# Kernel tuning notes

Hardware: AMD Instinct MI355X
Metric: run time of the kernel (lower is better)

The kernel has to match this reference:

```python
import jax, jax.numpy as jnp
import numpy as np
from jax import lax

V, E, Q, D = 100000, 300, 64, 4096
K = 5
NEG_SLOPE = 0.01


def setup_inputs() -> dict:
    key = jax.random.key(0)
    ks = jax.random.split(key, 16)
    return {
        "question": jax.random.randint(ks[0], (Q,), 0, V),
        "doc1": jax.random.randint(ks[1], (D,), 0, V),
        "doc2": jax.random.randint(ks[2], (D,), 0, V),
        "doc1_sim": jax.random.uniform(ks[3], (D, Q), dtype=jnp.float32),
        "doc2_sim": jax.random.uniform(ks[4], (D, Q), dtype=jnp.float32),
        "gaf": jax.random.normal(ks[5], (4,), dtype=jnp.float32),
        "baf": jax.random.normal(ks[6], (4,), dtype=jnp.float32),
        "emb": jax.random.normal(ks[7], (V, E), dtype=jnp.float32) * 0.1,
        "idf": jax.random.uniform(ks[8], (V, 1), dtype=jnp.float32) * 10.0,
        "conv_w": jax.random.normal(ks[9], (E, E, 3), dtype=jnp.float32) * (1.0 / np.sqrt(3 * E)),
        "conv_b": jax.random.normal(ks[10], (E,), dtype=jnp.float32) * 0.01,
        "qw_w": jax.random.normal(ks[11], (1, E + 1), dtype=jnp.float32) * (1.0 / np.sqrt(E + 1)),
        "qw_b": jax.random.normal(ks[12], (1,), dtype=jnp.float32) * 0.01,
        "lin1_w": jax.random.normal(ks[13], (8, 6), dtype=jnp.float32) * (1.0 / np.sqrt(6)),
        "lin2_w": jax.random.normal(ks[14], (1, 8), dtype=jnp.float32) * (1.0 / np.sqrt(8)),
        "out_w": jax.random.normal(ks[15], (1, 5), dtype=jnp.float32) * (1.0 / np.sqrt(5)),
    }


def _leaky(x):
    return jnp.where(x >= 0, x, NEG_SLOPE * x)


def _conv_residual(x, w, b):
    # x: [L, E]. Torch Conv1d(E,E,3,padding=2) followed by slice [1:L+1] is a
    # centered SAME conv; activation applied before the residual add.
    y = lax.conv_general_dilated(x.T[None], w, (1,), [(1, 1)],
                                 dimension_numbers=("NCW", "OIW", "NCW"))
    y = y[0] + b[:, None]            # [E, L]
    return _leaky(y).T + x           # [L, E]


def _cosine(A, B):
    # A: [Q, E], B: [L, E] -> [Q, L]
    num = A @ B.T
    den = jnp.linalg.norm(A, axis=-1)[:, None] * jnp.linalg.norm(B, axis=-1)[None, :]
    return num / den


def _kmax_pool(sim):
    # sim: [Q, L] -> [Q, 2] = (max, mean of top-K)
    top = lax.top_k(sim, K)[0]       # descending [Q, K]
    return jnp.stack([top[:, 0], jnp.mean(top, axis=-1)], axis=-1)


def _get_output(pooled_list, q_weights, lin1_w, lin2_w):
    temp = jnp.concatenate(pooled_list, axis=-1)     # [Q, 6]
    lo = _leaky(temp @ lin1_w.T) @ lin2_w.T          # [Q, 1]
    lo = lo[:, 0] * q_weights
    return jnp.sum(lo) / lo.shape[0]


def reference(question, doc1, doc2, doc1_sim, doc2_sim, gaf, baf,
              emb, idf, conv_w, conv_b, qw_w, qw_b, lin1_w, lin2_w, out_w):
    q_emb = emb[question]            # [Q, E]
    d1_emb = emb[doc1]               # [D, E]
    d2_emb = emb[doc2]

    sim_ins_d1 = _cosine(q_emb, d1_emb)
    sim_ins_d2 = _cosine(q_emb, d2_emb)

    q_conv = _conv_residual(q_emb, conv_w, conv_b)
    d1_conv = _conv_residual(d1_emb, conv_w, conv_b)
    d2_conv = _conv_residual(d2_emb, conv_w, conv_b)

    sim_sen_d1 = _cosine(q_conv, d1_conv)
    sim_sen_d2 = _cosine(q_conv, d2_conv)

    sim_oh_d1 = doc1_sim.T           # [Q, D]
    sim_oh_d2 = doc2_sim.T

    p_oh_d1, p_ins_d1, p_sen_d1 = _kmax_pool(sim_oh_d1), _kmax_pool(sim_ins_d1), _kmax_pool(sim_sen_d1)
    p_oh_d2, p_ins_d2, p_sen_d2 = _kmax_pool(sim_oh_d2), _kmax_pool(sim_ins_d2), _kmax_pool(sim_sen_d2)

    q_idfs = idf[question]           # [Q, 1]
    qw = jnp.concatenate([q_conv, q_idfs], axis=-1) @ qw_w.T + qw_b  # [Q, 1]
    q_weights = jax.nn.softmax(qw[:, 0], axis=-1)

    doc1_emit = _get_output([p_oh_d1, p_ins_d1, p_sen_d1], q_weights, lin1_w, lin2_w)
    doc2_emit = _get_output([p_oh_d2, p_ins_d2, p_sen_d2], q_weights, lin1_w, lin2_w)

    good_feats = jnp.concatenate([gaf, doc1_emit[None]])  # [5]
    bad_feats = jnp.concatenate([baf, doc2_emit[None]])
    good_out = out_w @ good_feats                          # [1]
    bad_out = out_w @ bad_feats

    loss1 = jnp.mean(jnp.maximum(0.0, -(good_out - bad_out) + 1.0))
    return (loss1, good_out, bad_out, loss1, loss1)
```

## Files before the change

kernel.cpp:

```cpp
#include <hip/hip_runtime.h>
#include <math.h>

#define EE 300
#define KP 320
#define LDSW 328
#define QQ 64
#define DD 4096
#define NEG 0.01f

typedef __attribute__((ext_vector_type(8))) short short8;
typedef __attribute__((ext_vector_type(4))) float f32x4;
typedef unsigned short ushort_t;

__device__ inline ushort_t f2bf(float f) {
  unsigned u = __builtin_bit_cast(unsigned, f);
  u += 0x7fff + ((u >> 16) & 1);
  return (ushort_t)(u >> 16);
}
__device__ inline float bf2f(ushort_t h) {
  return __builtin_bit_cast(float, (unsigned)h << 16);
}
__device__ inline void top5_insert(float* t, float v) {
  if (v > t[4]) {
    t[4] = v;
    #pragma unroll
    for (int j = 4; j > 0; --j)
      if (t[j] > t[j - 1]) { float tmp = t[j]; t[j] = t[j - 1]; t[j - 1] = tmp; }
  }
}

#define GATHER_ROWS (66 + 4098 + 4098)
#define GATHER_BLOCKS ((GATHER_ROWS + 3) / 4)
#define WT_BLOCKS 143
#define OHPOOL_BLOCKS 256
#define PREP_BLOCKS (GATHER_BLOCKS + WT_BLOCKS + OHPOOL_BLOCKS)

__global__ __launch_bounds__(256) void prep(
    const float* __restrict__ emb, const int* __restrict__ question,
    const int* __restrict__ doc1, const int* __restrict__ doc2,
    const float* __restrict__ conv_w,
    const float* __restrict__ doc1_sim, const float* __restrict__ doc2_sim,
    ushort_t* __restrict__ qbe, ushort_t* __restrict__ d1be, ushort_t* __restrict__ d2be,
    ushort_t* __restrict__ qbc, ushort_t* __restrict__ d1bc, ushort_t* __restrict__ d2bc,
    ushort_t* __restrict__ wt2,
    float* __restrict__ nq2, float* __restrict__ nd12, float* __restrict__ nd22,
    float* __restrict__ pt5) {
  __shared__ float strip[64][33];
  int b = blockIdx.x;
  int tid = threadIdx.x;
  int wv = tid >> 6, lane = tid & 63;
  if (b < GATHER_BLOCKS) {
    int g = b * 4 + wv;
    if (g >= GATHER_ROWS) return;
    int t, row;
    if (g < 66)             { t = 0; row = g; }
    else if (g < 66 + 4098) { t = 1; row = g - 66; }
    else                    { t = 2; row = g - 4164; }
    const int* idx = t == 0 ? question : (t == 1 ? doc1 : doc2);
    int L = t == 0 ? QQ : DD;
    ushort_t* be = t == 0 ? qbe : (t == 1 ? d1be : d2be);
    ushort_t* bc = t == 0 ? qbc : (t == 1 ? d1bc : d2bc);
    float* nrm2 = t == 0 ? nq2 : (t == 1 ? nd12 : nd22);
    const short8 z8 = (short8){0, 0, 0, 0, 0, 0, 0, 0};
    if (row == 0 || row == L + 1) {
      if (lane < 40) *(short8*)(be + (size_t)row * KP + lane * 8) = z8;
      return;
    }
    int r = row - 1;
    const float* src = emb + (size_t)idx[r] * EE;
    float ss = 0.f;
    if (lane < 37) {
      f32x4 v0 = *(const f32x4*)(src + lane * 8);
      f32x4 v1 = *(const f32x4*)(src + lane * 8 + 4);
      short8 hb;
      #pragma unroll
      for (int e = 0; e < 4; ++e) { hb[e] = (short)f2bf(v0[e]); ss += v0[e] * v0[e]; }
      #pragma unroll
      for (int e = 0; e < 4; ++e) { hb[4 + e] = (short)f2bf(v1[e]); ss += v1[e] * v1[e]; }
      *(short8*)(be + (size_t)row * KP + lane * 8) = hb;
    } else if (lane == 37) {
      f32x4 v0 = *(const f32x4*)(src + 296);
      short8 hb = z8;
      #pragma unroll
      for (int e = 0; e < 4; ++e) { hb[e] = (short)f2bf(v0[e]); ss += v0[e] * v0[e]; }
      *(short8*)(be + (size_t)row * KP + 296) = hb;
    } else if (lane < 40) {
      *(short8*)(be + (size_t)row * KP + lane * 8) = z8;
    }
    if (lane < 20) bc[(size_t)r * KP + 300 + lane] = 0;
    #pragma unroll
    for (int o = 32; o; o >>= 1) ss += __shfl_xor(ss, o);
    if (lane == 0) nrm2[r] = ss;
  } else if (b < GATHER_BLOCKS + WT_BLOCKS) {
    int f = (b - GATHER_BLOCKS) * 4 + wv;
    if (f >= 570) return;
    int ks = f % 10, n = (f / 10) % 19, tap = f / 190;
    int o = n * 16 + (lane & 15);
    int kbase = ks * 32 + (lane >> 4) * 8;
    ushort_t* dst = wt2 + (size_t)f * 512 + lane * 8;
    #pragma unroll
    for (int e = 0; e < 8; ++e) {
      int k = kbase + e;
      float v = (o < EE && k < EE) ? conv_w[((size_t)o * EE + k) * 3 + tap] : 0.f;
      dst[e] = f2bf(v);
    }
  } else {
    int ob = b - (GATHER_BLOCKS + WT_BLOCKS);
    int o = ob >> 7, chunk = ob & 127;
    int ps = o ? 3 : 0;
    const float* dsim = o ? doc2_sim : doc1_sim;
    int l0 = chunk * 32;
    int r = tid >> 3, q0 = (tid & 7) * 8;
    const float* srcp = dsim + (size_t)(l0 + r) * QQ + q0;
    f32x4 v0 = *(const f32x4*)srcp;
    f32x4 v1 = *(const f32x4*)(srcp + 4);
    #pragma unroll
    for (int e = 0; e < 4; ++e) strip[q0 + e][r] = v0[e];
    #pragma unroll
    for (int e = 0; e < 4; ++e) strip[q0 + 4 + e][r] = v1[e];
    __syncthreads();
    if (tid < 64) {
      float t5[5] = {-1e30f, -1e30f, -1e30f, -1e30f, -1e30f};
      #pragma unroll
      for (int l = 0; l < 32; ++l) top5_insert(t5, strip[tid][l]);
      float* dst = pt5 + (((size_t)ps * QQ + tid) * 128 + chunk) * 8;
      *(f32x4*)dst = (f32x4){t5[0], t5[1], t5[2], t5[3]};
      *(f32x4*)(dst + 4) = (f32x4){t5[4], -1e30f, -1e30f, -1e30f};
    }
  }
}

__global__ __launch_bounds__(256) void conv_mfma(
    const ushort_t* __restrict__ wt2, const float* __restrict__ bias,
    const float* __restrict__ qw_w,
    const ushort_t* __restrict__ qbe, const ushort_t* __restrict__ d1be,
    const ushort_t* __restrict__ d2be,
    ushort_t* __restrict__ qbc, ushort_t* __restrict__ d1bc,
    ushort_t* __restrict__ d2bc,
    float* __restrict__ nqcH, float* __restrict__ nd1cH, float* __restrict__ nd2cH,
    float* __restrict__ qwaccH) {
  __shared__ ushort_t lds[34 * LDSW];
  __shared__ float normbuf[4][32];
  __shared__ float qwbuf[4][32];
  int bx = blockIdx.x;
  int t, m0, yh;
  if (bx < 4) { t = 0; m0 = (bx >> 1) * 32; yh = bx & 1; }
  else {
    int i = bx - 4;
    t = 1 + (i >> 8);
    int j = i & 255;
    m0 = (j >> 1) * 32; yh = j & 1;
  }
  const ushort_t* be = t == 0 ? qbe : (t == 1 ? d1be : d2be);
  ushort_t* bc = t == 0 ? qbc : (t == 1 ? d1bc : d2bc);
  float* ncH = t == 0 ? nqcH : (t == 1 ? nd1cH : nd2cH);
  int ncs = t == 0 ? QQ : DD;
  int tid = threadIdx.x;
  for (int s = tid; s < 34 * 40; s += 256) {
    int row = s / 40, col = s - row * 40;
    *(short8*)(&lds[row * LDSW + col * 8]) =
        *(const short8*)(be + (size_t)(m0 + row) * KP + col * 8);
  }
  __syncthreads();
  int wv = tid >> 6, lane = tid & 63, mrow = lane & 15, g = lane >> 4;
  int nstart, ncnt;
  if (yh == 0) { nstart = (wv < 2) ? 3 * wv : 2 * wv + 2; ncnt = (wv < 2) ? 3 : 2; }
  else         { nstart = (wv == 0) ? 10 : 2 * wv + 11;   ncnt = (wv == 0) ? 3 : 2; }
  f32x4 acc[3][2];
  #pragma unroll
  for (int j = 0; j < 3; ++j)
    #pragma unroll
    for (int h = 0; h < 2; ++h) acc[j][h] = (f32x4){0.f, 0.f, 0.f, 0.f};

  for (int tap = 0; tap < 3; ++tap) {
    const ushort_t* alo = &lds[(mrow + tap) * LDSW + g * 8];
    #pragma unroll
    for (int ks = 0; ks < 10; ++ks) {
      short8 a0 = *(const short8*)(alo + ks * 32);
      short8 a1 = *(const short8*)(alo + 16 * LDSW + ks * 32);
      #pragma unroll
      for (int j = 0; j < 3; ++j) {
        if (j < ncnt) {
          short8 bfr = *(const short8*)(wt2 +
              (size_t)((tap * 19 + nstart + j) * 10 + ks) * 512 + lane * 8);
          acc[j][0] = __builtin_amdgcn_mfma_f32_16x16x32_bf16(a0, bfr, acc[j][0], 0, 0, 0);
          acc[j][1] = __builtin_amdgcn_mfma_f32_16x16x32_bf16(a1, bfr, acc[j][1], 0, 0, 0);
        }
      }
    }
  }
  float ss[2][4] = {{0.f,0.f,0.f,0.f},{0.f,0.f,0.f,0.f}};
  float yq[2][4] = {{0.f,0.f,0.f,0.f},{0.f,0.f,0.f,0.f}};
  #pragma unroll
  for (int j = 0; j < 3; ++j) {
    if (j < ncnt) {
      int col = (nstart + j) * 16 + mrow;
      if (col < EE) {
        float bcol = bias[col];
        float qwc = (t == 0) ? qw_w[col] : 0.f;
        #pragma unroll
        for (int h = 0; h < 2; ++h) {
          #pragma unroll
          for (int r = 0; r < 4; ++r) {
            int lrow = h * 16 + g * 4 + r;
            float y = acc[j][h][r] + bcol;
            y = (y >= 0.f) ? y : NEG * y;
            y += bf2f(lds[(1 + lrow) * LDSW + col]);
            bc[(size_t)(m0 + lrow) * KP + col] = f2bf(y);
            ss[h][r] += y * y;
            if (t == 0) yq[h][r] += y * qwc;
          }
        }
      }
    }
  }
  #pragma unroll
  for (int h = 0; h < 2; ++h) {
    #pragma unroll
    for (int r = 0; r < 4; ++r) {
      float s = ss[h][r];
      s += __shfl_xor(s, 1); s += __shfl_xor(s, 2);
      s += __shfl_xor(s, 4); s += __shfl_xor(s, 8);
      float sq = yq[h][r];
      sq += __shfl_xor(sq, 1); sq += __shfl_xor(sq, 2);
      sq += __shfl_xor(sq, 4); sq += __shfl_xor(sq, 8);
      if (mrow == 0) {
        normbuf[wv][h * 16 + g * 4 + r] = s;
        qwbuf[wv][h * 16 + g * 4 + r] = sq;
      }
    }
  }
  __syncthreads();
  if (tid < 32) {
    ncH[(size_t)yh * ncs + m0 + tid] =
        normbuf[0][tid] + normbuf[1][tid] + normbuf[2][tid] + normbuf[3][tid];
    if (t == 0)
      qwaccH[yh * QQ + m0 + tid] =
          qwbuf[0][tid] + qwbuf[1][tid] + qwbuf[2][tid] + qwbuf[3][tid];
  }
}

__global__ __launch_bounds__(256) void sim_pool(
    const ushort_t* __restrict__ qbe, const ushort_t* __restrict__ d1be,
    const ushort_t* __restrict__ d2be,
    const ushort_t* __restrict__ qbc, const ushort_t* __restrict__ d1bc,
    const ushort_t* __restrict__ d2bc,
    const float* __restrict__ nq2, const float* __restrict__ nd12,
    const float* __restrict__ nd22, const float* __restrict__ nqcH,
    const float* __restrict__ nd1cH, const float* __restrict__ nd2cH,
    float* __restrict__ pt5) {
  __shared__ ushort_t ldsB[32 * LDSW];
  __shared__ float strip[64][33];
  int s = blockIdx.x >> 7, chunk = blockIdx.x & 127;
  int ps = (s == 0) ? 1 : (s == 1) ? 4 : (s == 2) ? 2 : 5;
  int l0 = chunk * 32;
  const ushort_t* A = (s < 2) ? qbe + KP : qbc;
  const ushort_t* B = s == 0 ? d1be + KP : s == 1 ? d2be + KP
                    : s == 2 ? d1bc : d2bc;
  int tid = threadIdx.x;
  for (int i = tid; i < 32 * 40; i += 256) {
    int row = i / 40, col = i - row * 40;
    *(short8*)(&ldsB[row * LDSW + col * 8]) =
        *(const short8*)(B + (size_t)(l0 + row) * KP + col * 8);
  }
  __syncthreads();
  int wv = tid >> 6, lane = tid & 63, mrow = lane & 15, g = lane >> 4;
  f32x4 acc[2];
  acc[0] = (f32x4){0.f, 0.f, 0.f, 0.f};
  acc[1] = (f32x4){0.f, 0.f, 0.f, 0.f};
  const ushort_t* arow = A + (size_t)(wv * 16 + mrow) * KP + g * 8;
  #pragma unroll
  for (int ks = 0; ks < 10; ++ks) {
    short8 a = *(const short8*)(arow + ks * 32);
    #pragma unroll
    for (int n = 0; n < 2; ++n) {
      short8 bfr = *(const short8*)(&ldsB[(n * 16 + mrow) * LDSW + g * 8 + ks * 32]);
      acc[n] = __builtin_amdgcn_mfma_f32_16x16x32_bf16(a, bfr, acc[n], 0, 0, 0);
    }
  }
  #pragma unroll
  for (int n = 0; n < 2; ++n) {
    int l = n * 16 + mrow;
    float nb2v = (s == 0) ? nd12[l0 + l]
               : (s == 1) ? nd22[l0 + l]
               : (s == 2) ? (nd1cH[l0 + l] + nd1cH[DD + l0 + l])
                          : (nd2cH[l0 + l] + nd2cH[DD + l0 + l]);
    float inb = rsqrtf(nb2v);
    #pragma unroll
    for (int r = 0; r < 4; ++r) {
      int q = wv * 16 + g * 4 + r;
      float na2v = (s < 2) ? nq2[q] : (nqcH[q] + nqcH[QQ + q]);
      strip[q][l] = acc[n][r] * rsqrtf(na2v) * inb;
    }
  }
  __syncthreads();
  if (tid < 64) {
    float t5[5] = {-1e30f, -1e30f, -1e30f, -1e30f, -1e30f};
    #pragma unroll
    for (int l = 0; l < 32; ++l) top5_insert(t5, strip[tid][l]);
    float* dst = pt5 + (((size_t)ps * QQ + tid) * 128 + chunk) * 8;
    *(f32x4*)dst = (f32x4){t5[0], t5[1], t5[2], t5[3]};
    *(f32x4*)(dst + 4) = (f32x4){t5[4], -1e30f, -1e30f, -1e30f};
  }
}

__global__ __launch_bounds__(256) void merge(
    const float* __restrict__ pt5, float* __restrict__ pool) {
  int widx = blockIdx.x * 4 + (threadIdx.x >> 6);
  int lane = threadIdx.x & 63;
  int src = widx >> 6, q = widx & 63;
  const float* p0 = pt5 + (((size_t)src * QQ + q) * 128 + 2 * lane) * 8;
  float t5[5] = {-1e30f, -1e30f, -1e30f, -1e30f, -1e30f};
  #pragma unroll
  for (int c = 0; c < 2; ++c)
    #pragma unroll
    for (int j = 0; j < 5; ++j) top5_insert(t5, p0[c * 8 + j]);
  #pragma unroll
  for (int mask = 1; mask < 64; mask <<= 1) {
    float a[5], bb[5];
    #pragma unroll
    for (int j = 0; j < 5; ++j) { a[j] = t5[j]; bb[j] = __shfl_xor(t5[j], mask); }
    int ia = 0, ib = 0;
    #pragma unroll
    for (int j = 0; j < 5; ++j) t5[j] = (a[ia] >= bb[ib]) ? a[ia++] : bb[ib++];
  }
  if (lane == 0) {
    float sm = t5[0] + t5[1] + t5[2] + t5[3] + t5[4];
    pool[((size_t)src * QQ + q) * 2 + 0] = t5[0];
    pool[((size_t)src * QQ + q) * 2 + 1] = sm * 0.2f;
  }
}

__global__ void final_kernel(
    const float* __restrict__ qwaccH, const float* __restrict__ idf,
    const int* __restrict__ question, const float* __restrict__ qw_w,
    const float* __restrict__ qw_b, const float* __restrict__ pool,
    const float* __restrict__ lin1_w, const float* __restrict__ lin2_w,
    const float* __restrict__ out_w, const float* __restrict__ gaf,
    const float* __restrict__ baf, float* __restrict__ out5) {
  int q = threadIdx.x;
  float s = qwaccH[q] + qwaccH[QQ + q] + qw_b[0] + idf[question[q]] * qw_w[EE];
  float m = s;
  #pragma unroll
  for (int o = 32; o; o >>= 1) m = fmaxf(m, __shfl_xor(m, o));
  float e = expf(s - m);
  float se = e;
  #pragma unroll
  for (int o = 32; o; o >>= 1) se += __shfl_xor(se, o);
  float qwgt = e / se;

  float emit[2];
  for (int doc = 0; doc < 2; ++doc) {
    float temp[6];
    #pragma unroll
    for (int j = 0; j < 3; ++j) {
      temp[2 * j]     = pool[(((size_t)doc * 3 + j) * QQ + q) * 2 + 0];
      temp[2 * j + 1] = pool[(((size_t)doc * 3 + j) * QQ + q) * 2 + 1];
    }
    float lo = 0.f;
    #pragma unroll
    for (int r = 0; r < 8; ++r) {
      float h = 0.f;
      #pragma unroll
      for (int c = 0; c < 6; ++c) h += lin1_w[r * 6 + c] * temp[c];
      h = (h >= 0.f) ? h : NEG * h;
      lo += lin2_w[r] * h;
    }
    lo *= qwgt;
    #pragma unroll
    for (int o = 32; o; o >>= 1) lo += __shfl_xor(lo, o);
    emit[doc] = lo / (float)QQ;
  }
  if (q == 0) {
    float good = out_w[0] * gaf[0] + out_w[1] * gaf[1] + out_w[2] * gaf[2] +
                 out_w[3] * gaf[3] + out_w[4] * emit[0];
    float bad  = out_w[0] * baf[0] + out_w[1] * baf[1] + out_w[2] * baf[2] +
                 out_w[3] * baf[3] + out_w[4] * emit[1];
    float l1 = fmaxf(0.f, -(good - bad) + 1.f);
    out5[0] = l1; out5[1] = good; out5[2] = bad; out5[3] = l1; out5[4] = l1;
  }
}

extern "C" void kernel_launch(void* const* d_in, const int* in_sizes, int n_in,
                              void* d_out, int out_size, void* d_ws, size_t ws_size,
                              hipStream_t stream) {
  (void)in_sizes; (void)n_in; (void)out_size; (void)ws_size;
  const int* question   = (const int*)d_in[0];
  const int* doc1       = (const int*)d_in[1];
  const int* doc2       = (const int*)d_in[2];
  const float* doc1_sim = (const float*)d_in[3];
  const float* doc2_sim = (const float*)d_in[4];
  const float* gaf      = (const float*)d_in[5];
  const float* baf      = (const float*)d_in[6];
  const float* emb      = (const float*)d_in[7];
  const float* idf      = (const float*)d_in[8];
  const float* conv_w   = (const float*)d_in[9];
  const float* conv_b   = (const float*)d_in[10];
  const float* qw_w     = (const float*)d_in[11];
  const float* qw_b     = (const float*)d_in[12];
  const float* lin1_w   = (const float*)d_in[13];
  const float* lin2_w   = (const float*)d_in[14];
  const float* out_w    = (const float*)d_in[15];
  float* out = (float*)d_out;

  char* p = (char*)d_ws;
  ushort_t* qbe  = (ushort_t*)p; p += (size_t)(QQ + 2) * KP * 2;
  ushort_t* d1be = (ushort_t*)p; p += (size_t)(DD + 2) * KP * 2;
  ushort_t* d2be = (ushort_t*)p; p += (size_t)(DD + 2) * KP * 2;
  ushort_t* qbc  = (ushort_t*)p; p += (size_t)QQ * KP * 2;
  ushort_t* d1bc = (ushort_t*)p; p += (size_t)DD * KP * 2;
  ushort_t* d2bc = (ushort_t*)p; p += (size_t)DD * KP * 2;
  ushort_t* wt2  = (ushort_t*)p; p += (size_t)570 * 512 * 2;
  float* nq2    = (float*)p; p += QQ * 4;
  float* nd12   = (float*)p; p += DD * 4;
  float* nd22   = (float*)p; p += DD * 4;
  float* nqcH   = (float*)p; p += 2 * QQ * 4;
  float* nd1cH  = (float*)p; p += 2 * DD * 4;
  float* nd2cH  = (float*)p; p += 2 * DD * 4;
  float* qwaccH = (float*)p; p += 2 * QQ * 4;
  float* pt5    = (float*)p; p += (size_t)6 * QQ * 128 * 8 * 4;
  float* pool   = (float*)p; p += 6 * QQ * 2 * 4;

  prep<<<PREP_BLOCKS, 256, 0, stream>>>(
      emb, question, doc1, doc2, conv_w, doc1_sim, doc2_sim,
      qbe, d1be, d2be, qbc, d1bc, d2bc, wt2,
      nq2, nd12, nd22, pt5);

  conv_mfma<<<516, 256, 0, stream>>>(
      wt2, conv_b, qw_w, qbe, d1be, d2be, qbc, d1bc, d2bc,
      nqcH, nd1cH, nd2cH, qwaccH);

  sim_pool<<<512, 256, 0, stream>>>(
      qbe, d1be, d2be, qbc, d1bc, d2bc,
      nq2, nd12, nd22, nqcH, nd1cH, nd2cH, pt5);

  merge<<<96, 256, 0, stream>>>(pt5, pool);

  final_kernel<<<1, 64, 0, stream>>>(qwaccH, idf, question, qw_w, qw_b, pool,
                                     lin1_w, lin2_w, out_w, gaf, baf, out);
}
```

Before: 59.01 us.

## Retile conv MFMA blocks to 64 rows by quarter of output columns

The conv kernel now gives each block 64 sequence rows and one quarter of the output channels (5 N-tiles) instead of 32 rows and half the channels. Each wave reuses every weight fragment across four row tiles, which cuts global weight reads per MFMA, at the cost of one wave carrying a fifth tile alone and so an imbalanced load. Partial norm and qw sums are now split into four pieces that downstream kernels add together. LDS use grows to hold 66 rows.

Measured after the change: 61.77 us. +4.7%, slower.

```diff
diff --git a/kernel.cpp b/kernel.cpp
--- a/kernel.cpp
+++ b/kernel.cpp
@@ -137,69 +137,74 @@
     const ushort_t* __restrict__ d2be,
     ushort_t* __restrict__ qbc, ushort_t* __restrict__ d1bc,
     ushort_t* __restrict__ d2bc,
-    float* __restrict__ nqcH, float* __restrict__ nd1cH, float* __restrict__ nd2cH,
-    float* __restrict__ qwaccH) {
-  __shared__ ushort_t lds[34 * LDSW];
-  __shared__ float normbuf[4][32];
-  __shared__ float qwbuf[4][32];
+    float* __restrict__ nqcQ, float* __restrict__ nd1cQ, float* __restrict__ nd2cQ,
+    float* __restrict__ qwaccQ) {
+  __shared__ ushort_t lds[66 * LDSW];
+  __shared__ float normbuf[4][64];
+  __shared__ float qwbuf[4][64];
   int bx = blockIdx.x;
-  int t, m0, yh;
-  if (bx < 4) { t = 0; m0 = (bx >> 1) * 32; yh = bx & 1; }
+  int t, m0, yq;
+  if (bx < 4) { t = 0; m0 = 0; yq = bx; }
   else {
     int i = bx - 4;
     t = 1 + (i >> 8);
     int j = i & 255;
-    m0 = (j >> 1) * 32; yh = j & 1;
+    m0 = (j >> 2) * 64; yq = j & 3;
   }
   const ushort_t* be = t == 0 ? qbe : (t == 1 ? d1be : d2be);
   ushort_t* bc = t == 0 ? qbc : (t == 1 ? d1bc : d2bc);
-  float* ncH = t == 0 ? nqcH : (t == 1 ? nd1cH : nd2cH);
-  int ncs = t == 0 ? QQ : DD;
+  float* ncQ = t == 0 ? nqcQ : (t == 1 ? nd1cQ : nd2cQ);
+  int L = t == 0 ? QQ : DD;
   int tid = threadIdx.x;
-  for (int s = tid; s < 34 * 40; s += 256) {
+  for (int s = tid; s < 66 * 40; s += 256) {
     int row = s / 40, col = s - row * 40;
     *(short8*)(&lds[row * LDSW + col * 8]) =
         *(const short8*)(be + (size_t)(m0 + row) * KP + col * 8);
   }
   __syncthreads();
   int wv = tid >> 6, lane = tid & 63, mrow = lane & 15, g = lane >> 4;
-  int nstart, ncnt;
-  if (yh == 0) { nstart = (wv < 2) ? 3 * wv : 2 * wv + 2; ncnt = (wv < 2) ? 3 : 2; }
-  else         { nstart = (wv == 0) ? 10 : 2 * wv + 11;   ncnt = (wv == 0) ? 3 : 2; }
-  f32x4 acc[3][2];
-  #pragma unroll
-  for (int j = 0; j < 3; ++j)
-    #pragma unroll
-    for (int h = 0; h < 2; ++h) acc[j][h] = (f32x4){0.f, 0.f, 0.f, 0.f};
+  int nt0 = yq * 5 + wv;
+  int nt1 = yq * 5 + 4;
+  bool v1 = (wv == 0) && (nt1 <= 18);
+  f32x4 acc[2][4];
+  #pragma unroll
+  for (int j = 0; j < 2; ++j)
+    #pragma unroll
+    for (int h = 0; h < 4; ++h) acc[j][h] = (f32x4){0.f, 0.f, 0.f, 0.f};
 
   for (int tap = 0; tap < 3; ++tap) {
     const ushort_t* alo = &lds[(mrow + tap) * LDSW + g * 8];
     #pragma unroll
     for (int ks = 0; ks < 10; ++ks) {
-      short8 a0 = *(const short8*)(alo + ks * 32);
-      short8 a1 = *(const short8*)(alo + 16 * LDSW + ks * 32);
-      #pragma unroll
-      for (int j = 0; j < 3; ++j) {
-        if (j < ncnt) {
-          short8 bfr = *(const short8*)(wt2 +
-              (size_t)((tap * 19 + nstart + j) * 10 + ks) * 512 + lane * 8);
-          acc[j][0] = __builtin_amdgcn_mfma_f32_16x16x32_bf16(a0, bfr, acc[j][0], 0, 0, 0);
-          acc[j][1] = __builtin_amdgcn_mfma_f32_16x16x32_bf16(a1, bfr, acc[j][1], 0, 0, 0);
-        }
+      short8 a[4];
+      #pragma unroll
+      for (int h = 0; h < 4; ++h)
+        a[h] = *(const short8*)(alo + h * 16 * LDSW + ks * 32);
+      short8 b0 = *(const short8*)(wt2 +
+          (size_t)((tap * 19 + nt0) * 10 + ks) * 512 + lane * 8);
+      #pragma unroll
+      for (int h = 0; h < 4; ++h)
+        acc[0][h] = __builtin_amdgcn_mfma_f32_16x16x32_bf16(a[h], b0, acc[0][h], 0, 0, 0);
+      if (v1) {
+        short8 b1 = *(const short8*)(wt2 +
+            (size_t)((tap * 19 + nt1) * 10 + ks) * 512 + lane * 8);
+        #pragma unroll
+        for (int h = 0; h < 4; ++h)
+          acc[1][h] = __builtin_amdgcn_mfma_f32_16x16x32_bf16(a[h], b1, acc[1][h], 0, 0, 0);
       }
     }
   }
-  float ss[2][4] = {{0.f,0.f,0.f,0.f},{0.f,0.f,0.f,0.f}};
-  float yq[2][4] = {{0.f,0.f,0.f,0.f},{0.f,0.f,0.f,0.f}};
-  #pragma unroll
-  for (int j = 0; j < 3; ++j) {
-    if (j < ncnt) {
-      int col = (nstart + j) * 16 + mrow;
+  float ss[4][4] = {{0.f},{0.f},{0.f},{0.f}};
+  float yqd[4][4] = {{0.f},{0.f},{0.f},{0.f}};
+  #pragma unroll
+  for (int j = 0; j < 2; ++j) {
+    if (j == 0 || v1) {
+      int col = (j == 0 ? nt0 : nt1) * 16 + mrow;
       if (col < EE) {
         float bcol = bias[col];
         float qwc = (t == 0) ? qw_w[col] : 0.f;
         #pragma unroll
-        for (int h = 0; h < 2; ++h) {
+        for (int h = 0; h < 4; ++h) {
           #pragma unroll
           for (int r = 0; r < 4; ++r) {
             int lrow = h * 16 + g * 4 + r;
@@ -208,20 +213,20 @@
             y += bf2f(lds[(1 + lrow) * LDSW + col]);
             bc[(size_t)(m0 + lrow) * KP + col] = f2bf(y);
             ss[h][r] += y * y;
-            if (t == 0) yq[h][r] += y * qwc;
+            if (t == 0) yqd[h][r] += y * qwc;
           }
         }
       }
     }
   }
   #pragma unroll
-  for (int h = 0; h < 2; ++h) {
+  for (int h = 0; h < 4; ++h) {
     #pragma unroll
     for (int r = 0; r < 4; ++r) {
       float s = ss[h][r];
       s += __shfl_xor(s, 1); s += __shfl_xor(s, 2);
       s += __shfl_xor(s, 4); s += __shfl_xor(s, 8);
-      float sq = yq[h][r];
+      float sq = yqd[h][r];
       sq += __shfl_xor(sq, 1); sq += __shfl_xor(sq, 2);
       sq += __shfl_xor(sq, 4); sq += __shfl_xor(sq, 8);
       if (mrow == 0) {
@@ -231,11 +236,11 @@
     }
   }
   __syncthreads();
-  if (tid < 32) {
-    ncH[(size_t)yh * ncs + m0 + tid] =
+  if (tid < 64) {
+    ncQ[(size_t)yq * L + m0 + tid] =
         normbuf[0][tid] + normbuf[1][tid] + normbuf[2][tid] + normbuf[3][tid];
     if (t == 0)
-      qwaccH[yh * QQ + m0 + tid] =
+      qwaccQ[yq * QQ + tid] =
           qwbuf[0][tid] + qwbuf[1][tid] + qwbuf[2][tid] + qwbuf[3][tid];
   }
 }
@@ -246,8 +251,8 @@
     const ushort_t* __restrict__ qbc, const ushort_t* __restrict__ d1bc,
     const ushort_t* __restrict__ d2bc,
     const float* __restrict__ nq2, const float* __restrict__ nd12,
-    const float* __restrict__ nd22, const float* __restrict__ nqcH,
-    const float* __restrict__ nd1cH, const float* __restrict__ nd2cH,
+    const float* __restrict__ nd22, const float* __restrict__ nqcQ,
+    const float* __restrict__ nd1cQ, const float* __restrict__ nd2cQ,
     float* __restrict__ pt5) {
   __shared__ ushort_t ldsB[32 * LDSW];
   __shared__ float strip[64][33];
@@ -281,15 +286,19 @@
   #pragma unroll
   for (int n = 0; n < 2; ++n) {
     int l = n * 16 + mrow;
-    float nb2v = (s == 0) ? nd12[l0 + l]
-               : (s == 1) ? nd22[l0 + l]
-               : (s == 2) ? (nd1cH[l0 + l] + nd1cH[DD + l0 + l])
-                          : (nd2cH[l0 + l] + nd2cH[DD + l0 + l]);
+    float nb2v;
+    if (s == 0)      nb2v = nd12[l0 + l];
+    else if (s == 1) nb2v = nd22[l0 + l];
+    else if (s == 2) nb2v = nd1cQ[l0 + l] + nd1cQ[DD + l0 + l] +
+                            nd1cQ[2 * DD + l0 + l] + nd1cQ[3 * DD + l0 + l];
+    else             nb2v = nd2cQ[l0 + l] + nd2cQ[DD + l0 + l] +
+                            nd2cQ[2 * DD + l0 + l] + nd2cQ[3 * DD + l0 + l];
     float inb = rsqrtf(nb2v);
     #pragma unroll
     for (int r = 0; r < 4; ++r) {
       int q = wv * 16 + g * 4 + r;
-      float na2v = (s < 2) ? nq2[q] : (nqcH[q] + nqcH[QQ + q]);
+      float na2v = (s < 2) ? nq2[q]
+                 : (nqcQ[q] + nqcQ[QQ + q] + nqcQ[2 * QQ + q] + nqcQ[3 * QQ + q]);
       strip[q][l] = acc[n][r] * rsqrtf(na2v) * inb;
     }
   }
@@ -332,14 +341,15 @@
 }
 
 __global__ void final_kernel(
-    const float* __restrict__ qwaccH, const float* __restrict__ idf,
+    const float* __restrict__ qwaccQ, const float* __restrict__ idf,
     const int* __restrict__ question, const float* __restrict__ qw_w,
     const float* __restrict__ qw_b, const float* __restrict__ pool,
     const float* __restrict__ lin1_w, const float* __restrict__ lin2_w,
     const float* __restrict__ out_w, const float* __restrict__ gaf,
     const float* __restrict__ baf, float* __restrict__ out5) {
   int q = threadIdx.x;
-  float s = qwaccH[q] + qwaccH[QQ + q] + qw_b[0] + idf[question[q]] * qw_w[EE];
+  float s = qwaccQ[q] + qwaccQ[QQ + q] + qwaccQ[2 * QQ + q] + qwaccQ[3 * QQ + q] +
+            qw_b[0] + idf[question[q]] * qw_w[EE];
   float m = s;
   #pragma unroll
   for (int o = 32; o; o >>= 1) m = fmaxf(m, __shfl_xor(m, o));
@@ -414,10 +424,10 @@
   float* nq2    = (float*)p; p += QQ * 4;
   float* nd12   = (float*)p; p += DD * 4;
   float* nd22   = (float*)p; p += DD * 4;
-  float* nqcH   = (float*)p; p += 2 * QQ * 4;
-  float* nd1cH  = (float*)p; p += 2 * DD * 4;
-  float* nd2cH  = (float*)p; p += 2 * DD * 4;
-  float* qwaccH = (float*)p; p += 2 * QQ * 4;
+  float* nqcQ   = (float*)p; p += 4 * QQ * 4;
+  float* nd1cQ  = (float*)p; p += 4 * DD * 4;
+  float* nd2cQ  = (float*)p; p += 4 * DD * 4;
+  float* qwaccQ = (float*)p; p += 4 * QQ * 4;
   float* pt5    = (float*)p; p += (size_t)6 * QQ * 128 * 8 * 4;
   float* pool   = (float*)p; p += 6 * QQ * 2 * 4;
 
@@ -428,14 +438,14 @@
 
   conv_mfma<<<516, 256, 0, stream>>>(
       wt2, conv_b, qw_w, qbe, d1be, d2be, qbc, d1bc, d2bc,
-      nqcH, nd1cH, nd2cH, qwaccH);
+      nqcQ, nd1cQ, nd2cQ, qwaccQ);
 
   sim_pool<<<512, 256, 0, stream>>>(
       qbe, d1be, d2be, qbc, d1bc, d2bc,
-      nq2, nd12, nd22, nqcH, nd1cH, nd2cH, pt5);
+      nq2, nd12, nd22, nqcQ, nd1cQ, nd2cQ, pt5);
 
   merge<<<96, 256, 0, stream>>>(pt5, pool);
 
-  final_kernel<<<1, 64, 0, stream>>>(qwaccH, idf, question, qw_w, qw_b, pool,
+  final_kernel<<<1, 64, 0, stream>>>(qwaccQ, idf, question, qw_w, qw_b, pool,
                                      lin1_w, lin2_w, out_w, gaf, baf, out);
 }
```
